# Kernel tuning notes

Measured on AMD Instinct MI355X. Metric: run time of the kernel, lower is better.

The kernel has to match this reference:

```python
import jax, jax.numpy as jnp
import numpy as np

B, N, CT = 64, 256, 3
HID, HEADS = 256, 4
C = HID // HEADS          # per-head channels
E = 8192                  # number of edges
NEG = 0.2                 # GATv2 leaky_relu negative slope
EPS_BN = 1e-5


def setup_inputs() -> dict:
    key = jax.random.key(0)
    ks = jax.random.split(key, 32)
    F_in = N * CT
    s1 = 1.0 / np.sqrt(F_in)
    sh = 1.0 / np.sqrt(HID)
    inp = {
        "x": jax.random.normal(ks[0], (B, N, N, CT), jnp.float32),
        "edge_index": jax.random.randint(ks[1], (2, E), 0, N, dtype=jnp.int32),
        # node_proj: Linear + BatchNorm1d (eval) params
        "W1": jax.random.normal(ks[2], (F_in, HID), jnp.float32) * s1,
        "b1": jnp.zeros((HID,), jnp.float32),
        "g1": jnp.ones((HID,), jnp.float32),
        "be1": jnp.zeros((HID,), jnp.float32),
        "m1": jnp.zeros((HID,), jnp.float32),
        "v1": jnp.ones((HID,), jnp.float32),
        # GATv2 layer 0
        "Wl0": jax.random.normal(ks[3], (HID, HID), jnp.float32) * sh,
        "bl0": jnp.zeros((HID,), jnp.float32),
        "Wr0": jax.random.normal(ks[4], (HID, HID), jnp.float32) * sh,
        "br0": jnp.zeros((HID,), jnp.float32),
        "att0": jax.random.normal(ks[5], (HEADS, C), jnp.float32) * (1.0 / np.sqrt(C)),
        "bo0": jnp.zeros((HID,), jnp.float32),
        # GATv2 layer 1
        "Wl1": jax.random.normal(ks[6], (HID, HID), jnp.float32) * sh,
        "bl1": jnp.zeros((HID,), jnp.float32),
        "Wr1": jax.random.normal(ks[7], (HID, HID), jnp.float32) * sh,
        "br1": jnp.zeros((HID,), jnp.float32),
        "att1": jax.random.normal(ks[8], (HEADS, C), jnp.float32) * (1.0 / np.sqrt(C)),
        "bo1": jnp.zeros((HID,), jnp.float32),
        # output_proj: Linear + BatchNorm1d (eval) params
        "W2": jax.random.normal(ks[9], (HID, HID), jnp.float32) * sh,
        "b2": jnp.zeros((HID,), jnp.float32),
        "g2": jnp.ones((HID,), jnp.float32),
        "be2": jnp.zeros((HID,), jnp.float32),
        "m2": jnp.zeros((HID,), jnp.float32),
        "v2": jnp.ones((HID,), jnp.float32),
    }
    return inp


def _bn(x, g, b, m, v):
    # BatchNorm1d in eval mode: per-feature affine with running stats
    return (x - m) * jax.lax.rsqrt(v + EPS_BN) * g + b


def _gatv2(h, src, dst, Wl, bl, Wr, br, att, bo):
    # h: (N, HID). GATv2Conv (PyG semantics): lin_l on source, lin_r on target.
    xl = (h @ Wl + bl).reshape(N, HEADS, C)
    xr = (h @ Wr + br).reshape(N, HEADS, C)
    x_j = xl[src]                        # (E, H, C) source features
    x_i = xr[dst]                        # (E, H, C) target features
    e = jax.nn.leaky_relu(x_i + x_j, NEG)
    logits = jnp.einsum('ehc,hc->eh', e, att)          # (E, H)
    mx = jax.ops.segment_max(logits, dst, num_segments=N)
    a = jnp.exp(logits - mx[dst])
    den = jax.ops.segment_sum(a, dst, num_segments=N)
    a = a / (den[dst] + 1e-16)                         # neighborhood softmax
    out = jax.ops.segment_sum(x_j * a[:, :, None], dst, num_segments=N)
    return out.reshape(N, HID) + bo


def reference(x, edge_index, W1, b1, g1, be1, m1, v1,
              Wl0, bl0, Wr0, br0, att0, bo0,
              Wl1, bl1, Wr1, br1, att1, bo1,
              W2, b2, g2, be2, m2, v2):
    gelu = lambda t: jax.nn.gelu(t, approximate=False)
    xf = x.reshape(B, N, N * CT)
    # node_proj (eval: dropout off, BN uses running stats -> vmappable)
    h = gelu(_bn(xf @ W1 + b1, g1, be1, m1, v1))       # (B, N, HID)
    src, dst = edge_index[0], edge_index[1]

    def per_sample(hn):
        h0 = gelu(_gatv2(hn, src, dst, Wl0, bl0, Wr0, br0, att0, bo0))
        h1 = gelu(_gatv2(h0, src, dst, Wl1, bl1, Wr1, br1, att1, bo1))
        return h1.mean(axis=0)                          # mean over nodes

    pooled = jax.vmap(per_sample)(h)                    # (B, HID)
    return gelu(_bn(pooled @ W2 + b2, g2, be2, m2, v2))
```

## Files before the change

### kernel.cpp

```cpp
#include <hip/hip_runtime.h>
#include <hip/hip_bf16.h>
#include <math.h>

#define BATCH   64
#define NNODES  256
#define HID     256
#define HEADS   4
#define CDIM    64
#define NEDGES  8192
#define NEG_SLOPE 0.2f
#define EPS_BN 1e-5f


typedef __bf16 bf16_t;
typedef __bf16 bf16x8 __attribute__((ext_vector_type(8)));
typedef float  f32x4  __attribute__((ext_vector_type(4)));

__device__ __forceinline__ float gelu_f(float x) {
    return 0.5f * x * (1.0f + erff(x * 0.70710678118654752440f));
}

#define SWZ(r, c) ((c) ^ ((r) & 3) ^ (((r) >> 2) & 3))

__global__ __launch_bounds__(256) void prep_kernel(
        const int* __restrict__ ei,
        const float* __restrict__ W1, const float* __restrict__ Wa,
        const float* __restrict__ Wb, const float* __restrict__ Wc,
        const float* __restrict__ Wd,
        int* __restrict__ noff, int* __restrict__ csrc,
        bf16_t* __restrict__ T1, bf16_t* __restrict__ Ta,
        bf16_t* __restrict__ Tb, bf16_t* __restrict__ Tc,
        bf16_t* __restrict__ Td) {
    const int bx = blockIdx.x;
    const int tid = threadIdx.x;
    if (bx == 448) {
        __shared__ int cnt[NNODES];
        __shared__ int off_s[NNODES + 1];
        cnt[tid] = 0;
        __syncthreads();
        for (int e = tid; e < NEDGES; e += 256) atomicAdd(&cnt[ei[NEDGES + e]], 1);
        __syncthreads();
        if (tid == 0) {
            int s = 0;
            for (int i = 0; i < NNODES; ++i) { off_s[i] = s; s += cnt[i]; }
            off_s[NNODES] = s;
        }
        __syncthreads();
        cnt[tid] = off_s[tid];
        noff[tid] = off_s[tid];
        if (tid == 0) noff[NNODES] = off_s[NNODES];
        __syncthreads();
        for (int e = tid; e < NEDGES; e += 256) {
            int d = ei[NEDGES + e];
            int p = atomicAdd(&cnt[d], 1);
            csrc[p] = ei[e];
        }
        return;
    }
    __shared__ float tile[32][33];
    const float* in; bf16_t* out; int K, t;
    if (bx < 192) { in = W1; out = T1; K = 768; t = bx; }
    else {
        int r = bx - 192, mid = r >> 6; t = r & 63; K = 256;
        if (mid == 0) { in = Wa; out = Ta; }
        else if (mid == 1) { in = Wb; out = Tb; }
        else if (mid == 2) { in = Wc; out = Tc; }
        else { in = Wd; out = Td; }
    }
    const int kt = t >> 3, nt = t & 7;
    const int k0 = kt * 32, n0 = nt * 32;
    const int x = tid & 31, y = tid >> 5;
    #pragma unroll
    for (int j = 0; j < 4; ++j)
        tile[y + j * 8][x] = in[(size_t)(k0 + y + j * 8) * 256 + n0 + x];
    __syncthreads();
    #pragma unroll
    for (int j = 0; j < 4; ++j)
        out[(size_t)(n0 + y + j * 8) * K + k0 + x] = (bf16_t)tile[x][y + j * 8];
}

template<int A_F32, int DUAL, int EPI_BN, int PERM>
__global__ __launch_bounds__(256, 4) void gemm_kernel(
        const void* __restrict__ Ap,
        const bf16_t* __restrict__ Bt0, const bf16_t* __restrict__ Bt1,
        bf16_t* __restrict__ C0p, bf16_t* __restrict__ C1p, int K,
        const float* __restrict__ bias0, const float* __restrict__ bias1,
        const float* __restrict__ g, const float* __restrict__ be,
        const float* __restrict__ mu, const float* __restrict__ var) {
    __shared__ bf16_t As[32 * 32];
    __shared__ bf16_t Bs[256 * 32];
    const int tid  = threadIdx.x;
    const int lane = tid & 63;
    const int wv   = tid >> 6;
    const int mblk = blockIdx.y * 32;
    const bool second = DUAL && (blockIdx.x == 1);
    const bf16_t* Bt = second ? Bt1 : Bt0;
    bf16_t* Cp = second ? C1p : C0p;
    const float* bias = second ? bias1 : bias0;

    f32x4 acc[2][4];
    #pragma unroll
    for (int f = 0; f < 2; ++f)
        #pragma unroll
        for (int t = 0; t < 4; ++t) acc[f][t] = (f32x4){0.f, 0.f, 0.f, 0.f};

    const int arow = tid >> 2;
    const int achk = tid & 3;
    const int gr   = mblk + arow;
    const int arr  = PERM ? ((gr & 63) * 256 + (gr >> 6)) : gr;
    const int fm   = lane & 15, q = lane >> 4;

    for (int k0 = 0; k0 < K; k0 += 32) {
        if (tid < 128) {
            bf16x8 v;
            if (A_F32) {
                const float* ap = (const float*)Ap + (size_t)arr * K + k0 + achk * 8;
                f32x4 a0 = *(const f32x4*)ap;
                f32x4 a1 = *(const f32x4*)(ap + 4);
                #pragma unroll
                for (int j = 0; j < 4; ++j) { v[j] = (bf16_t)a0[j]; v[4 + j] = (bf16_t)a1[j]; }
            } else {
                v = *(const bf16x8*)((const bf16_t*)Ap + (size_t)arr * K + k0 + achk * 8);
            }
            *(bf16x8*)(&As[(arow * 4 + SWZ(arow, achk)) * 8]) = v;
        }
        {
            const bf16_t* bp = Bt + (size_t)tid * K + k0;
            bf16x8 b0 = *(const bf16x8*)bp;
            bf16x8 b1 = *(const bf16x8*)(bp + 8);
            bf16x8 b2 = *(const bf16x8*)(bp + 16);
            bf16x8 b3 = *(const bf16x8*)(bp + 24);
            *(bf16x8*)(&Bs[(tid * 4 + SWZ(tid, 0)) * 8]) = b0;
            *(bf16x8*)(&Bs[(tid * 4 + SWZ(tid, 1)) * 8]) = b1;
            *(bf16x8*)(&Bs[(tid * 4 + SWZ(tid, 2)) * 8]) = b2;
            *(bf16x8*)(&Bs[(tid * 4 + SWZ(tid, 3)) * 8]) = b3;
        }
        __syncthreads();

        bf16x8 af[2], bfv[4];
        #pragma unroll
        for (int f = 0; f < 2; ++f) {
            const int r = f * 16 + fm;
            af[f] = *(const bf16x8*)(&As[(r * 4 + SWZ(r, q)) * 8]);
        }
        #pragma unroll
        for (int t = 0; t < 4; ++t) {
            const int n = wv * 64 + t * 16 + fm;
            bfv[t] = *(const bf16x8*)(&Bs[(n * 4 + SWZ(n, q)) * 8]);
        }
        #pragma unroll
        for (int f = 0; f < 2; ++f)
            #pragma unroll
            for (int t = 0; t < 4; ++t)
                acc[f][t] = __builtin_amdgcn_mfma_f32_16x16x32_bf16(
                    af[f], bfv[t], acc[f][t], 0, 0, 0);
        __syncthreads();
    }

    const int quad = lane >> 4, cn = lane & 15;
    #pragma unroll
    for (int t = 0; t < 4; ++t) {
        const int n = wv * 64 + t * 16 + cn;
        const float bv = bias[n];
        float scale = 1.0f, shift = 0.0f;
        if (EPI_BN) {
            float s = g[n] * rsqrtf(var[n] + EPS_BN);
            scale = s;
            shift = be[n] - mu[n] * s;
        }
        #pragma unroll
        for (int f = 0; f < 2; ++f) {
            #pragma unroll
            for (int r = 0; r < 4; ++r) {
                const int m = mblk + f * 16 + quad * 4 + r;
                float val = acc[f][t][r] + bv;
                if (EPI_BN) val = gelu_f(val * scale + shift);
                Cp[(size_t)m * 256 + n] = (bf16_t)val;
            }
        }
    }
}

__global__ __launch_bounds__(256) void edge_kernel(
        const bf16_t* __restrict__ XL, const bf16_t* __restrict__ XR,
        const float* __restrict__ att, const float* __restrict__ bo,
        const int* __restrict__ noff, const int* __restrict__ csrc,
        bf16_t* __restrict__ Hout) {
    const int bid  = blockIdx.x;
    const int i    = bid >> 3;
    const int tid  = threadIdx.x;
    const int w    = tid >> 6;
    const int lane = tid & 63;
    const int bg   = lane >> 3;
    const int cg   = lane & 7;
    const int b    = (bid & 7) * 8 + bg;
    const int cbase = w * CDIM + cg * 8;
    const size_t orow = ((size_t)i * BATCH + b) * HID + cbase;
    const float* bor = bo + cbase;

    const int s0 = noff[i], s1 = noff[i + 1];
    if (s0 == s1) {
        bf16x8 ov;
        #pragma unroll
        for (int q = 0; q < 8; ++q) ov[q] = (bf16_t)gelu_f(bor[q]);
        *(bf16x8*)(Hout + orow) = ov;
        return;
    }

    float a6[8], a4[8], xi[8];
    {
        const float* ar = att + cbase;
        const bf16x8 xr = *(const bf16x8*)(XR + orow);
        #pragma unroll
        for (int q = 0; q < 8; ++q) {
            float a = ar[q];
            a6[q] = 0.6f * a; a4[q] = 0.4f * a;
            xi[q] = (float)xr[q];
        }
    }

    const bf16_t* XLb = XL + (size_t)b * HID + cbase;
    const size_t RSTR = (size_t)BATCH * HID;

    float mA = -1e30f, dA = 0.f, mB = -1e30f, dB = 0.f;
    float accA[8], accB[8];
    #pragma unroll
    for (int q = 0; q < 8; ++q) { accA[q] = 0.f; accB[q] = 0.f; }

    int jA = csrc[s0];
    int jB = csrc[(s0 + 1 < s1) ? s0 + 1 : s0];
    bf16x8 xA = *(const bf16x8*)(XLb + (size_t)jA * RSTR);
    bf16x8 xB = *(const bf16x8*)(XLb + (size_t)jB * RSTR);

    for (int e = s0; e < s1; e += 2) {
        const int nA = (e + 2 < s1) ? e + 2 : s0;
        const int nB = (e + 3 < s1) ? e + 3 : s0;
        const int jnA = csrc[nA], jnB = csrc[nB];
        const bf16x8 xnA = *(const bf16x8*)(XLb + (size_t)jnA * RSTR);
        const bf16x8 xnB = *(const bf16x8*)(XLb + (size_t)jnB * RSTR);

        float fA[8], fB[8];
        #pragma unroll
        for (int q = 0; q < 8; ++q) { fA[q] = (float)xA[q]; fB[q] = (float)xB[q]; }
        float pA = 0.f, pB = 0.f;
        #pragma unroll
        for (int q = 0; q < 8; ++q) {
            const float zA = xi[q] + fA[q];
            const float zB = xi[q] + fB[q];
            pA = fmaf(a6[q], zA, pA);
            pB = fmaf(a6[q], zB, pB);
            pA = fmaf(a4[q], __builtin_fabsf(zA), pA);
            pB = fmaf(a4[q], __builtin_fabsf(zB), pB);
        }
        pA += __shfl_xor(pA, 1, 64);  pB += __shfl_xor(pB, 1, 64);
        pA += __shfl_xor(pA, 2, 64);  pB += __shfl_xor(pB, 2, 64);
        pA += __shfl_xor(pA, 4, 64);  pB += __shfl_xor(pB, 4, 64);

        const float mnA = fmaxf(mA, pA);
        const float alA = __expf(mA - mnA);
        const float wA  = __expf(pA - mnA);
        const float vB  = (e + 1 < s1) ? 1.f : 0.f;
        const float mnB = fmaxf(mB, pB);
        const float alB = __expf(mB - mnB);
        const float wB  = __expf(pB - mnB) * vB;
        dA = dA * alA + wA;
        dB = dB * alB + wB;
        #pragma unroll
        for (int q = 0; q < 8; ++q) {
            accA[q] = fmaf(accA[q], alA, wA * fA[q]);
            accB[q] = fmaf(accB[q], alB, wB * fB[q]);
        }
        mA = mnA; mB = mnB;
        xA = xnA; xB = xnB;
    }

    const float mm = fmaxf(mA, mB);
    const float g1 = __expf(mA - mm);
    const float g2 = __expf(mB - mm);
    const float inv = 1.0f / (dA * g1 + dB * g2 + 1e-16f);
    bf16x8 ov;
    #pragma unroll
    for (int q = 0; q < 8; ++q) {
        const float o = (accA[q] * g1 + accB[q] * g2) * inv + bor[q];
        ov[q] = (bf16_t)gelu_f(o);
    }
    *(bf16x8*)(Hout + orow) = ov;
}

__global__ __launch_bounds__(256) void pf_kernel(
        const bf16_t* __restrict__ H1, const float* __restrict__ W2,
        const float* __restrict__ b2, const float* __restrict__ g2,
        const float* __restrict__ be2, const float* __restrict__ m2,
        const float* __restrict__ v2, float* __restrict__ out) {
    __shared__ float pl[HID];
    const int b = blockIdx.x, f = threadIdx.x;
    float s = 0.f;
    for (int n = 0; n < NNODES; ++n)
        s += (float)H1[((size_t)n * BATCH + b) * HID + f];
    pl[f] = s * (1.0f / (float)NNODES);
    __syncthreads();
    float acc = 0.f;
    for (int k = 0; k < HID; ++k) acc += pl[k] * W2[(size_t)k * HID + f];
    acc += b2[f];
    const float scale = g2[f] * rsqrtf(v2[f] + EPS_BN);
    acc = (acc - m2[f]) * scale + be2[f];
    out[b * HID + f] = gelu_f(acc);
}

extern "C" void kernel_launch(void* const* d_in, const int* in_sizes, int n_in,
                              void* d_out, int out_size, void* d_ws, size_t ws_size,
                              hipStream_t stream) {
    const float* x    = (const float*)d_in[0];
    const int*   ei   = (const int*)d_in[1];
    const float* W1   = (const float*)d_in[2];
    const float* b1   = (const float*)d_in[3];
    const float* g1   = (const float*)d_in[4];
    const float* be1  = (const float*)d_in[5];
    const float* m1   = (const float*)d_in[6];
    const float* v1   = (const float*)d_in[7];
    const float* Wl0  = (const float*)d_in[8];
    const float* bl0  = (const float*)d_in[9];
    const float* Wr0  = (const float*)d_in[10];
    const float* br0  = (const float*)d_in[11];
    const float* att0 = (const float*)d_in[12];
    const float* bo0  = (const float*)d_in[13];
    const float* Wl1  = (const float*)d_in[14];
    const float* bl1  = (const float*)d_in[15];
    const float* Wr1  = (const float*)d_in[16];
    const float* br1  = (const float*)d_in[17];
    const float* att1 = (const float*)d_in[18];
    const float* bo1  = (const float*)d_in[19];
    const float* W2   = (const float*)d_in[20];
    const float* b2   = (const float*)d_in[21];
    const float* g2   = (const float*)d_in[22];
    const float* be2  = (const float*)d_in[23];
    const float* m2   = (const float*)d_in[24];
    const float* v2   = (const float*)d_in[25];

    char* ws = (char*)d_ws;
    const int M = BATCH * NNODES;
    const size_t SZ_BF = (size_t)M * HID * sizeof(bf16_t);

    int*    noff = (int*)ws;                ws += 2048;
    int*    csrc = (int*)ws;                ws += 32768;
    bf16_t* W1t  = (bf16_t*)ws;             ws += 256 * 768 * 2;
    bf16_t* Wl0t = (bf16_t*)ws;             ws += 256 * 256 * 2;
    bf16_t* Wr0t = (bf16_t*)ws;             ws += 256 * 256 * 2;
    bf16_t* Wl1t = (bf16_t*)ws;             ws += 256 * 256 * 2;
    bf16_t* Wr1t = (bf16_t*)ws;             ws += 256 * 256 * 2;
    bf16_t* H    = (bf16_t*)ws;             ws += SZ_BF;
    bf16_t* H2   = (bf16_t*)ws;             ws += SZ_BF;
    bf16_t* XL   = (bf16_t*)ws;             ws += SZ_BF;
    bf16_t* XR   = (bf16_t*)ws;             ws += SZ_BF;

    prep_kernel<<<449, 256, 0, stream>>>(ei, W1, Wl0, Wr0, Wl1, Wr1,
                                         noff, csrc, W1t, Wl0t, Wr0t, Wl1t, Wr1t);

    gemm_kernel<1, 0, 1, 1><<<dim3(1, 512), 256, 0, stream>>>(
        x, W1t, nullptr, H, nullptr, 768, b1, nullptr, g1, be1, m1, v1);

    gemm_kernel<0, 1, 0, 0><<<dim3(2, 512), 256, 0, stream>>>(
        H, Wl0t, Wr0t, XL, XR, 256, bl0, br0, nullptr, nullptr, nullptr, nullptr);
    edge_kernel<<<NNODES * 8, 256, 0, stream>>>(XL, XR, att0, bo0, noff, csrc, H2);

    gemm_kernel<0, 1, 0, 0><<<dim3(2, 512), 256, 0, stream>>>(
        H2, Wl1t, Wr1t, XL, XR, 256, bl1, br1, nullptr, nullptr, nullptr, nullptr);
    edge_kernel<<<NNODES * 8, 256, 0, stream>>>(XL, XR, att1, bo1, noff, csrc, H);

    pf_kernel<<<BATCH, 256, 0, stream>>>(H, W2, b2, g2, be2, m2, v2, (float*)d_out);
}
```

Before: 321.7 us.

## Store transposed weights as K-panels for coalesced B loads, widen LDS swizzle

The prep kernel now writes the bf16 transposed weights in a panel layout, with each 32-wide K slice stored contiguously as 256x32. The GEMM loads each B tile as one contiguous 16KB panel so that consecutive threads read consecutive 16-byte chunks, replacing the strided per-row loads used before. The LDS swizzle gains a third XOR term to cut bank conflicts under the new store pattern. The gain depends on whether the B loads were limited by uncoalesced access, and the layout change must stay consistent across every GEMM that reads these weights.

```diff
diff --git a/kernel.cpp b/kernel.cpp
--- a/kernel.cpp
+++ b/kernel.cpp
@@ -20,7 +20,7 @@
     return 0.5f * x * (1.0f + erff(x * 0.70710678118654752440f));
 }
 
-#define SWZ(r, c) ((c) ^ ((r) & 3) ^ (((r) >> 2) & 3))
+#define SWZ(r, c) ((c) ^ ((r) & 3) ^ (((r) >> 2) & 3) ^ (((r) >> 4) & 3))
 
 __global__ __launch_bounds__(256) void prep_kernel(
         const int* __restrict__ ei,
@@ -58,10 +58,10 @@
         return;
     }
     __shared__ float tile[32][33];
-    const float* in; bf16_t* out; int K, t;
-    if (bx < 192) { in = W1; out = T1; K = 768; t = bx; }
+    const float* in; bf16_t* out; int t;
+    if (bx < 192) { in = W1; out = T1; t = bx; }
     else {
-        int r = bx - 192, mid = r >> 6; t = r & 63; K = 256;
+        int r = bx - 192, mid = r >> 6; t = r & 63;
         if (mid == 0) { in = Wa; out = Ta; }
         else if (mid == 1) { in = Wb; out = Tb; }
         else if (mid == 2) { in = Wc; out = Tc; }
@@ -75,8 +75,10 @@
         tile[y + j * 8][x] = in[(size_t)(k0 + y + j * 8) * 256 + n0 + x];
     __syncthreads();
     #pragma unroll
-    for (int j = 0; j < 4; ++j)
-        out[(size_t)(n0 + y + j * 8) * K + k0 + x] = (bf16_t)tile[x][y + j * 8];
+    for (int j = 0; j < 4; ++j) {
+        const int n = n0 + y + j * 8;
+        out[((size_t)kt * 256 + n) * 32 + x] = (bf16_t)tile[x][y + j * 8];
+    }
 }
 
 template<int A_F32, int DUAL, int EPI_BN, int PERM>
@@ -125,15 +127,14 @@
             *(bf16x8*)(&As[(arow * 4 + SWZ(arow, achk)) * 8]) = v;
         }
         {
-            const bf16_t* bp = Bt + (size_t)tid * K + k0;
-            bf16x8 b0 = *(const bf16x8*)bp;
-            bf16x8 b1 = *(const bf16x8*)(bp + 8);
-            bf16x8 b2 = *(const bf16x8*)(bp + 16);
-            bf16x8 b3 = *(const bf16x8*)(bp + 24);
-            *(bf16x8*)(&Bs[(tid * 4 + SWZ(tid, 0)) * 8]) = b0;
-            *(bf16x8*)(&Bs[(tid * 4 + SWZ(tid, 1)) * 8]) = b1;
-            *(bf16x8*)(&Bs[(tid * 4 + SWZ(tid, 2)) * 8]) = b2;
-            *(bf16x8*)(&Bs[(tid * 4 + SWZ(tid, 3)) * 8]) = b3;
+            const bf16_t* panel = Bt + (size_t)(k0 >> 5) * (256 * 32);
+            #pragma unroll
+            for (int c = 0; c < 4; ++c) {
+                const int f = c * 256 + tid;
+                const bf16x8 bv = *(const bf16x8*)(panel + (size_t)f * 8);
+                const int n = f >> 2, kc = f & 3;
+                *(bf16x8*)(&Bs[(n * 4 + SWZ(n, kc)) * 8]) = bv;
+            }
         }
         __syncthreads();
 
```

Result: faster. 297.1 us (-7.6%).
